# Kernel tuning notes

Hardware: AMD Instinct MI355X
Metric: run time of the kernel (lower is better)

## Reference

```python
import jax, jax.numpy as jnp
import numpy as np

N0, N1, N2 = 100000, 25000, 6250
F = 128
OUT = 5


def _mean_agg(feat_src, src, dst, n_dst):
    # DGL copy_u + mean: segment mean over destination nodes (0 for isolated dst)
    s = jax.ops.segment_sum(feat_src[src], dst, num_segments=n_dst)
    cnt = jax.ops.segment_sum(jnp.ones_like(dst, dtype=feat_src.dtype), dst, num_segments=n_dst)
    return s / jnp.maximum(cnt, 1.0)[:, None]


def _graph_conv(feat, src, dst, W, b, n):
    # DGL GraphConv, norm='both': D_src^-1/2 gather-sum D_dst^-1/2, then linear
    dt = feat.dtype
    out_deg = jax.ops.segment_sum(jnp.ones_like(src, dtype=dt), src, num_segments=n)
    in_deg = jax.ops.segment_sum(jnp.ones_like(dst, dtype=dt), dst, num_segments=n)
    ns = jnp.where(out_deg > 0, out_deg ** -0.5, 0.0)
    nd = jnp.where(in_deg > 0, in_deg ** -0.5, 0.0)
    agg = jax.ops.segment_sum((feat * ns[:, None])[src], dst, num_segments=n)
    return (agg * nd[:, None]) @ W + b


def setup_inputs() -> dict:
    key = jax.random.key(0)
    keys = jax.random.split(key, 64)
    _c = iter(range(64))
    def nrm(shape, s=0.05):
        return jax.random.normal(keys[next(_c)], shape, dtype=jnp.float32) * s
    def ri(n, hi):
        return jax.random.randint(keys[next(_c)], (n,), 0, hi)
    inp = {
        'X': nrm((N0, 32), 1.0),
        'g0_src': ri(1600000, N0), 'g0_dst': ri(1600000, N0),
        'g1_src': ri(400000, N1), 'g1_dst': ri(400000, N1),
        'g2_src': ri(100000, N2), 'g2_dst': ri(100000, N2),
        'inc0_src': ri(100000, N0), 'inc0_dst': ri(100000, N1),
        'inc1_src': ri(25000, N1), 'inc1_dst': ri(25000, N2),
        'dec0_src': ri(100000, N2), 'dec0_dst': ri(100000, N1),
        'dec1_src': ri(400000, N1), 'dec1_dst': ri(400000, N0),
        'W_emb': nrm((32, F)), 'b_emb': jnp.zeros((F,), jnp.float32),
        'W_gcn0': nrm((F, F)), 'b_gcn0': jnp.zeros((F,), jnp.float32),
        'W_gcn1': nrm((F, F)), 'b_gcn1': jnp.zeros((F,), jnp.float32),
        'W_gcn2': nrm((F, F)), 'b_gcn2': jnp.zeros((F,), jnp.float32),
        'W_enc0': nrm((F, F)), 'b_enc0': jnp.zeros((F,), jnp.float32),
        'W_enc1': nrm((F, F)), 'b_enc1': jnp.zeros((F,), jnp.float32),
        'W_dec0': nrm((F, F)), 'b_dec0': jnp.zeros((F,), jnp.float32),
        'W_dec1': nrm((F, F)), 'b_dec1': jnp.zeros((F,), jnp.float32),
        'W_head0': nrm((2 * F, OUT)), 'b_head0': jnp.zeros((OUT,), jnp.float32),
        'W_head1': nrm((2 * F, OUT)), 'b_head1': jnp.zeros((OUT,), jnp.float32),
        'W_head2': nrm((2 * F, OUT)), 'b_head2': jnp.zeros((OUT,), jnp.float32),
    }
    return inp


def reference(X, g0_src, g0_dst, g1_src, g1_dst, g2_src, g2_dst,
              inc0_src, inc0_dst, inc1_src, inc1_dst,
              dec0_src, dec0_dst, dec1_src, dec1_dst,
              W_emb, b_emb, W_gcn0, b_gcn0, W_gcn1, b_gcn1, W_gcn2, b_gcn2,
              W_enc0, b_enc0, W_enc1, b_enc1, W_dec0, b_dec0, W_dec1, b_dec1,
              W_head0, b_head0, W_head1, b_head1, W_head2, b_head2):
    # embedding at finest scale
    h0 = X @ W_emb + b_emb                                   # [N0, F]
    # encode + pool fine -> coarse (copy_u/mean)
    h1 = _mean_agg(h0 @ W_enc0 + b_enc0, inc0_src, inc0_dst, N1)   # [N1, F]
    h2 = _mean_agg(h1 @ W_enc1 + b_enc1, inc1_src, inc1_dst, N2)   # [N2, F]
    # intra-scale GraphConv
    g0 = _graph_conv(h0, g0_src, g0_dst, W_gcn0, b_gcn0, N0)
    g1 = _graph_conv(h1, g1_src, g1_dst, W_gcn1, b_gcn1, N1)
    g2 = _graph_conv(h2, g2_src, g2_dst, W_gcn2, b_gcn2, N2)
    # decode coarse -> fine
    d2 = g2
    d1 = _mean_agg(d2 @ W_dec0 + b_dec0, dec0_src, dec0_dst, N1)   # [N1, F]
    d0 = _mean_agg(d1 @ W_dec1 + b_dec1, dec1_src, dec1_dst, N0)   # [N0, F]
    # per-scale heads with softmax
    o0 = jax.nn.softmax(jnp.concatenate([g0, d0], -1) @ W_head0 + b_head0, axis=-1)
    o1 = jax.nn.softmax(jnp.concatenate([g1, d1], -1) @ W_head1 + b_head1, axis=-1)
    o2 = jax.nn.softmax(jnp.concatenate([g2, d2], -1) @ W_head2 + b_head2, axis=-1)
    return jnp.concatenate([o0, o1, o2], axis=0)             # [N0+N1+N2, OUT]
```

## Files before the change

### kernel.cpp

```cpp
#include <hip/hip_runtime.h>

#define F 128
static const int N0 = 100000, N1 = 25000, N2 = 6250;

typedef unsigned short u16;
typedef unsigned int   u32;
typedef __attribute__((ext_vector_type(8))) short bf16x8;
typedef __attribute__((ext_vector_type(4))) float f32x4;

__device__ __forceinline__ float bf2f(u16 u) {
    union { u32 i; float f; } v; v.i = ((u32)u) << 16; return v.f;
}
__device__ __forceinline__ u16 f2bf(float f) {
    u32 u = __float_as_uint(f);
    u += 0x7fff + ((u >> 16) & 1);
    return (u16)(u >> 16);
}

struct Seg7 {
    const int* src[7];
    const int* dst[7];
    int end[7];
    int cbase[7];
    int obase[7];
};
struct W7 { const float* w[7]; };

#define EPT 4
#define CEPT 8
#define SM32  (64*(32+8)*2 + 128*(32+8)*2 + 128*4)


__device__ __forceinline__ void dev_mm32(char* smem, const float* __restrict__ Ap,
                                         const float* __restrict__ W,
                                         const float* __restrict__ bias,
                                         u16* __restrict__ out, int M, int blk) {
    const int K = 32;
    const int KST = K + 8;
    u16* Al = (u16*)smem;
    u16* Wt = (u16*)(smem + 64 * KST * 2);
    float* bl = (float*)(smem + 64 * KST * 2 + 128 * KST * 2);
    int tid = threadIdx.x;
    int m0 = blk * 64;

    for (int i = tid; i < K * 128; i += 256) {
        int k = i >> 7, n = i & 127;
        Wt[n * KST + k] = f2bf(W[i]);
    }
    for (int i = tid; i < 64 * K; i += 256) {
        int r = i / K, c = i % K;
        int gr = m0 + r;
        Al[r * KST + c] = (gr < M) ? f2bf(Ap[(size_t)gr * K + c]) : (u16)0;
    }
    if (tid < 128) bl[tid] = bias[tid];
    __syncthreads();

    int w = tid >> 6, lane = tid & 63, m16 = lane & 15, quad = lane >> 4;
    f32x4 acc[8];
#pragma unroll
    for (int t = 0; t < 8; t++)
#pragma unroll
        for (int r = 0; r < 4; r++) acc[t][r] = 0.f;

    {
        bf16x8 af = *(const bf16x8*)&Al[(w * 16 + m16) * KST + quad * 8];
#pragma unroll
        for (int t = 0; t < 8; t++) {
            bf16x8 bf = *(const bf16x8*)&Wt[(t * 16 + m16) * KST + quad * 8];
            acc[t] = __builtin_amdgcn_mfma_f32_16x16x32_bf16(af, bf, acc[t], 0, 0, 0);
        }
    }
#pragma unroll
    for (int t = 0; t < 8; t++) {
#pragma unroll
        for (int r = 0; r < 4; r++) {
            int gr = m0 + w * 16 + quad * 4 + r;
            if (gr >= M) continue;
            int gc = t * 16 + m16;
            out[(size_t)gr * F + gc] = f2bf(acc[t][r] + bl[gc]);
        }
    }
}

template <bool MASK>
__device__ __forceinline__ void dev_mmd(const u16* __restrict__ Ap,
                                        const u16* __restrict__ Wtg,
                                        const float* __restrict__ bias,
                                        u16* __restrict__ out,
                                        const int* __restrict__ rowptr,
                                        int M, int blk) {
    int tid = threadIdx.x;
    int wv = tid >> 6, lane = tid & 63, m16 = lane & 15, quad = lane >> 4;
    int m0 = blk * 64;
    int arow = m0 + wv * 16 + m16;
    if (arow >= M) arow = M - 1;
    const u16* Arow = Ap + (size_t)arow * F;

    f32x4 acc[8];
#pragma unroll
    for (int t = 0; t < 8; t++)
#pragma unroll
        for (int r = 0; r < 4; r++) acc[t][r] = 0.f;

#pragma unroll
    for (int k0 = 0; k0 < F; k0 += 32) {
        bf16x8 af = *(const bf16x8*)&Arow[k0 + quad * 8];
#pragma unroll
        for (int t = 0; t < 8; t++) {
            bf16x8 bf = *(const bf16x8*)&Wtg[(t * 16 + m16) * F + k0 + quad * 8];
            acc[t] = __builtin_amdgcn_mfma_f32_16x16x32_bf16(af, bf, acc[t], 0, 0, 0);
        }
    }
#pragma unroll
    for (int t = 0; t < 8; t++) {
#pragma unroll
        for (int r = 0; r < 4; r++) {
            int gr = m0 + wv * 16 + quad * 4 + r;
            if (gr >= M) continue;
            int gc = t * 16 + m16;
            bool zrow = false;
            if (MASK) zrow = (rowptr[gr + 1] == rowptr[gr]);
            float v = acc[t][r] + bias[gc];
            out[(size_t)gr * F + gc] = zrow ? (u16)0 : f2bf(v);
        }
    }
}

template <int MODE>
__device__ __forceinline__ void dev_gather32(const u16* __restrict__ feat,
                                             const int* __restrict__ rowptr,
                                             const int* __restrict__ col,
                                             const int* __restrict__ od,
                                             u16* __restrict__ out, int M, int blk) {
    int row = (blk * 256 + (int)threadIdx.x) >> 5;
    if (row >= M) return;
    int l32 = threadIdx.x & 31;
    int fo = l32 << 2;
    int beg = rowptr[row], end = rowptr[row + 1];
    float a0 = 0.f, a1 = 0.f, a2 = 0.f, a3 = 0.f;
    int j = beg;
    for (; j + 8 <= end; j += 8) {
        int cc[8];
#pragma unroll
        for (int t = 0; t < 8; t++) cc[t] = col[j + t];
        float ss[8];
#pragma unroll
        for (int t = 0; t < 8; t++) {
            if (MODE == 1) { int o = od[cc[t]]; ss[t] = o > 0 ? rsqrtf((float)o) : 0.f; }
            else ss[t] = 1.f;
        }
        ushort4 uu[8];
#pragma unroll
        for (int t = 0; t < 8; t++) uu[t] = *(const ushort4*)&feat[(size_t)cc[t] * F + fo];
#pragma unroll
        for (int t = 0; t < 8; t++) {
            a0 += bf2f(uu[t].x) * ss[t]; a1 += bf2f(uu[t].y) * ss[t];
            a2 += bf2f(uu[t].z) * ss[t]; a3 += bf2f(uu[t].w) * ss[t];
        }
    }
    for (; j < end; j++) {
        int c = col[j];
        float s = 1.f;
        if (MODE == 1) { int o = od[c]; s = o > 0 ? rsqrtf((float)o) : 0.f; }
        ushort4 u = *(const ushort4*)&feat[(size_t)c * F + fo];
        a0 += bf2f(u.x) * s; a1 += bf2f(u.y) * s;
        a2 += bf2f(u.z) * s; a3 += bf2f(u.w) * s;
    }
    int deg = end - beg;
    float fs = (MODE == 0) ? (deg > 0 ? 1.f / (float)deg : 0.f)
                           : (deg > 0 ? rsqrtf((float)deg) : 0.f);
    ushort4 o;
    o.x = f2bf(a0 * fs); o.y = f2bf(a1 * fs);
    o.z = f2bf(a2 * fs); o.w = f2bf(a3 * fs);
    *(ushort4*)&out[(size_t)row * F + fo] = o;
}

template <bool GD>
__device__ __forceinline__ void dev_head(char* smem, const u16* __restrict__ g,
                                         const u16* __restrict__ d,
                                         const int* __restrict__ rowptr,
                                         const int* __restrict__ col,
                                         const float* __restrict__ Wh,
                                         const float* __restrict__ bh,
                                         float* __restrict__ out, int M, int blk) {
    float* Wl = (float*)smem;
    float* bl = (float*)(smem + 1280 * 4);
    int tid = threadIdx.x;
    for (int i = tid; i < 1280; i += 256) Wl[i] = Wh[i];
    if (tid < 5) bl[tid] = bh[tid];
    __syncthreads();

    int grp = tid >> 5;
    int l32 = tid & 31;
    int k0 = l32 << 2;
    for (int i = 0; i < 4; i++) {
        int row = blk * 32 + grp * 4 + i;
        if (row < M) {
            float dv[4];
            if (GD) {
                int beg = rowptr[row], end = rowptr[row + 1];
                dv[0] = dv[1] = dv[2] = dv[3] = 0.f;
                int j = beg;
                for (; j + 4 <= end; j += 4) {
                    int c0 = col[j], c1 = col[j + 1], c2 = col[j + 2], c3 = col[j + 3];
                    ushort4 u0 = *(const ushort4*)&d[(size_t)c0 * F + k0];
                    ushort4 u1 = *(const ushort4*)&d[(size_t)c1 * F + k0];
                    ushort4 u2 = *(const ushort4*)&d[(size_t)c2 * F + k0];
                    ushort4 u3 = *(const ushort4*)&d[(size_t)c3 * F + k0];
                    dv[0] += bf2f(u0.x) + bf2f(u1.x) + bf2f(u2.x) + bf2f(u3.x);
                    dv[1] += bf2f(u0.y) + bf2f(u1.y) + bf2f(u2.y) + bf2f(u3.y);
                    dv[2] += bf2f(u0.z) + bf2f(u1.z) + bf2f(u2.z) + bf2f(u3.z);
                    dv[3] += bf2f(u0.w) + bf2f(u1.w) + bf2f(u2.w) + bf2f(u3.w);
                }
                for (; j < end; j++) {
                    int c = col[j];
                    ushort4 u = *(const ushort4*)&d[(size_t)c * F + k0];
                    dv[0] += bf2f(u.x); dv[1] += bf2f(u.y);
                    dv[2] += bf2f(u.z); dv[3] += bf2f(u.w);
                }
                int deg = end - beg;
                float fs = deg > 0 ? 1.f / (float)deg : 0.f;
#pragma unroll
                for (int q = 0; q < 4; q++) dv[q] *= fs;
            } else {
                ushort4 du = *(const ushort4*)&d[(size_t)row * F + k0];
                dv[0] = bf2f(du.x); dv[1] = bf2f(du.y);
                dv[2] = bf2f(du.z); dv[3] = bf2f(du.w);
            }
            ushort4 gu = *(const ushort4*)&g[(size_t)row * F + k0];
            float gv[4] = {bf2f(gu.x), bf2f(gu.y), bf2f(gu.z), bf2f(gu.w)};
            float p[5];
#pragma unroll
            for (int o = 0; o < 5; o++) {
                float v = 0.f;
#pragma unroll
                for (int q = 0; q < 4; q++)
                    v += gv[q] * Wl[(k0 + q) * 5 + o] + dv[q] * Wl[(k0 + q + 128) * 5 + o];
                p[o] = v;
            }
#pragma unroll
            for (int o = 0; o < 5; o++) {
                float v = p[o];
                v += __shfl_xor(v, 16, 64);
                v += __shfl_xor(v, 8, 64);
                v += __shfl_xor(v, 4, 64);
                v += __shfl_xor(v, 2, 64);
                v += __shfl_xor(v, 1, 64);
                p[o] = v + bl[o];
            }
            if (l32 == 0) {
                float m = p[0];
#pragma unroll
                for (int o = 1; o < 5; o++) m = fmaxf(m, p[o]);
                float e[5], s = 0.f;
#pragma unroll
                for (int o = 0; o < 5; o++) { e[o] = expf(p[o] - m); s += e[o]; }
                float inv = 1.f / s;
#pragma unroll
                for (int o = 0; o < 5; o++) out[(size_t)row * 5 + o] = e[o] * inv;
            }
        }
    }
}


__global__ __launch_bounds__(256) void k_count_emb(Seg7 S, W7 Wsrc,
                                                   u16* __restrict__ WtAll,
                                                   int* __restrict__ cnt,
                                                   u16* __restrict__ occ, int ETOT,
                                                   const float* __restrict__ X,
                                                   const float* __restrict__ Wemb,
                                                   const float* __restrict__ bemb,
                                                   u16* __restrict__ h0,
                                                   int nbMM, int nbPrep) {
    __shared__ char smem[SM32];
    int blk = blockIdx.x;
    if (blk < nbMM) {
        dev_mm32(smem, X, Wemb, bemb, h0, N0, blk);
        return;
    }
    if (blk < nbMM + nbPrep) {
        int g = (blk - nbMM) * 256 + threadIdx.x;
        int m = g >> 14, idx = g & 16383;
        int n = idx >> 7, k = idx & 127;
        WtAll[g] = f2bf(Wsrc.w[m][k * 128 + n]);
        return;
    }
    int base = (blk - nbMM - nbPrep) * (256 * CEPT) + threadIdx.x;
    int ee[CEPT], grow[CEPT];
#pragma unroll
    for (int t = 0; t < CEPT; t++) {
        int e = base + t * 256;
        ee[t] = e;
        grow[t] = -1;
        if (e < ETOT) {
            int s = 0;
            while (e >= S.end[s]) s++;
            int le = e - ((s == 0) ? 0 : S.end[s - 1]);
            grow[t] = S.cbase[s] + S.dst[s][le];
        }
    }
    u32 r[CEPT];
#pragma unroll
    for (int t = 0; t < CEPT; t++)
        if (grow[t] >= 0) r[t] = atomicAdd((u32*)&cnt[grow[t]], 1u);
#pragma unroll
    for (int t = 0; t < CEPT; t++)
        if (grow[t] >= 0) occ[ee[t]] = (u16)r[t];
}

__global__ __launch_bounds__(256) void k_fill_od(Seg7 S,
                                                 const int* __restrict__ rowptr,
                                                 const u16* __restrict__ occ,
                                                 int* __restrict__ col,
                                                 int* __restrict__ od, int ETOT,
                                                 float invRow, float invOd) {
    int win = blockIdx.x & 7;
    int base = ((int)blockIdx.x >> 3) * (256 * EPT) + threadIdx.x;
#pragma unroll
    for (int t = 0; t < EPT; t++) {
        int e = base + t * 256;
        if (e >= ETOT) break;
        int s = 0;
        while (e >= S.end[s]) s++;
        int le = e - ((s == 0) ? 0 : S.end[s - 1]);
        int grow = S.cbase[s] + S.dst[s][le];
        int w1 = (int)((float)grow * invRow); w1 = w1 > 7 ? 7 : w1;
        int sv = -1;
        if (w1 == win || S.obase[s] >= 0) sv = S.src[s][le];
        if (w1 == win) col[rowptr[grow] + (int)occ[e]] = sv;
        if (S.obase[s] >= 0) {
            int gs = S.obase[s] + sv;
            int w2 = (int)((float)gs * invOd); w2 = w2 > 7 ? 7 : w2;
            if (w2 == win) atomicAdd(&od[gs], 1);
        }
    }
}

#define SCHUNK 4096
__global__ __launch_bounds__(1024) void k_scan1(const int* __restrict__ cnt,
                                                int* __restrict__ partial, int n) {
    __shared__ int red[1024];
    int tid = threadIdx.x;
    int base = blockIdx.x * SCHUNK + tid * 4;
    int s = 0;
#pragma unroll
    for (int j = 0; j < 4; j++) { int i = base + j; if (i < n) s += cnt[i]; }
    red[tid] = s;
    __syncthreads();
    for (int d = 512; d > 0; d >>= 1) {
        if (tid < d) red[tid] += red[tid + d];
        __syncthreads();
    }
    if (tid == 0) partial[blockIdx.x] = red[0];
}

__global__ __launch_bounds__(128) void k_scan2(int* __restrict__ partial, int G) {
    __shared__ int sh[128];
    int tid = threadIdx.x;
    sh[tid] = (tid < G) ? partial[tid] : 0;
    __syncthreads();
    for (int d = 1; d < 128; d <<= 1) {
        int t = (tid >= d) ? sh[tid - d] : 0;
        __syncthreads();
        sh[tid] += t;
        __syncthreads();
    }
    if (tid < G) partial[tid] = (tid > 0) ? sh[tid - 1] : 0;
    if (tid == 127) partial[G] = sh[127];
}

__global__ __launch_bounds__(1024) void k_scan3(const int* __restrict__ cnt,
                                                const int* __restrict__ partial,
                                                int* __restrict__ rowptr,
                                                int n, int G) {
    __shared__ int red[1024];
    int tid = threadIdx.x;
    int base = blockIdx.x * SCHUNK + tid * 4;
    int v0 = 0, v1 = 0, v2 = 0, v3 = 0;
    if (base + 0 < n) v0 = cnt[base + 0];
    if (base + 1 < n) v1 = cnt[base + 1];
    if (base + 2 < n) v2 = cnt[base + 2];
    if (base + 3 < n) v3 = cnt[base + 3];
    red[tid] = v0 + v1 + v2 + v3;
    __syncthreads();
    for (int d = 1; d < 1024; d <<= 1) {
        int t = (tid >= d) ? red[tid - d] : 0;
        __syncthreads();
        red[tid] += t;
        __syncthreads();
    }
    int off = partial[blockIdx.x] + ((tid > 0) ? red[tid - 1] : 0);
    if (base + 0 < n) { rowptr[base + 0] = off; off += v0; }
    if (base + 1 < n) { rowptr[base + 1] = off; off += v1; }
    if (base + 2 < n) { rowptr[base + 2] = off; off += v2; }
    if (base + 3 < n) { rowptr[base + 3] = off; off += v3; }
    if (blockIdx.x == 0 && tid == 0) rowptr[n] = partial[G];
}

template <int MODE>
__global__ __launch_bounds__(256) void k_g32(const u16* __restrict__ feat,
                                             const int* __restrict__ rowptr,
                                             const int* __restrict__ col,
                                             const int* __restrict__ od,
                                             u16* __restrict__ out, int M) {
    dev_gather32<MODE>(feat, rowptr, col, od, out, M, blockIdx.x);
}

template <int MA, int MB>
__global__ __launch_bounds__(256) void k_g32x2(
    const u16* fA, const int* rpA, const int* oA, u16* outA, int MAr, int nbA,
    const u16* fB, const int* rpB, const int* oB, u16* outB, int MBr,
    const int* __restrict__ col) {
    if ((int)blockIdx.x < nbA) dev_gather32<MA>(fA, rpA, col, oA, outA, MAr, blockIdx.x);
    else                       dev_gather32<MB>(fB, rpB, col, oB, outB, MBr, blockIdx.x - nbA);
}

template <bool MASK>
__global__ __launch_bounds__(256) void k_mmd(const u16* __restrict__ Ap,
                                             const u16* __restrict__ Wtg,
                                             const float* __restrict__ bias,
                                             u16* __restrict__ out,
                                             const int* __restrict__ rowptr, int M) {
    dev_mmd<MASK>(Ap, Wtg, bias, out, rowptr, M, blockIdx.x);
}

__global__ __launch_bounds__(256) void k_mmd2(
    const u16* A1, const u16* Wt1, const float* b1, u16* o1, const int* rp1, int M1, int nb1,
    const u16* A2, const u16* Wt2, const float* b2, u16* o2, int M2) {
    if ((int)blockIdx.x < nb1) dev_mmd<true >(A1, Wt1, b1, o1, rp1, M1, blockIdx.x);
    else                       dev_mmd<false>(A2, Wt2, b2, o2, nullptr, M2, blockIdx.x - nb1);
}

__global__ __launch_bounds__(256) void k_mmd_g32(
    const u16* A1, const u16* Wt1, const float* b1, u16* o1, const int* rp1, int M1, int nb1,
    const u16* feat, const int* rp2, const int* od2, u16* out2, int M2,
    const int* __restrict__ col) {
    if ((int)blockIdx.x < nb1) dev_mmd<true>(A1, Wt1, b1, o1, rp1, M1, blockIdx.x);
    else dev_gather32<1>(feat, rp2, col, od2, out2, M2, blockIdx.x - nb1);
}

__global__ __launch_bounds__(256) void k_g32_mmd(
    const u16* feat, const int* rp1, const int* od1, u16* out1, int M1, int nb1,
    const u16* A2, const u16* Wt2, const float* b2, u16* o2, int M2,
    const int* __restrict__ col) {
    if ((int)blockIdx.x < nb1) dev_gather32<1>(feat, rp1, col, od1, out1, M1, blockIdx.x);
    else dev_mmd<false>(A2, Wt2, b2, o2, nullptr, M2, blockIdx.x - nb1);
}

__global__ __launch_bounds__(256) void k_head3(
    const u16* Ga, const u16* dFeat, const int* rpD1, const int* colp,
    const float* Wa, const float* Ba, int nb0,
    const u16* Gb, const u16* Db, const float* Wb, const float* Bb, int nb1,
    const u16* Gc, const float* Wc, const float* Bc,
    float* __restrict__ out) {
    __shared__ char smem[1280 * 4 + 32];
    int b = blockIdx.x;
    if (b < nb0)            dev_head<true >(smem, Ga, dFeat, rpD1, colp, Wa, Ba, out, N0, b);
    else if (b < nb0 + nb1) dev_head<false>(smem, Gb, Db, nullptr, nullptr, Wb, Bb, out + (size_t)N0 * 5, N1, b - nb0);
    else                    dev_head<false>(smem, Gc, Gc, nullptr, nullptr, Wc, Bc, out + (size_t)(N0 + N1) * 5, N2, b - nb0 - nb1);
}

extern "C" void kernel_launch(void* const* d_in, const int* in_sizes, int n_in,
                              void* d_out, int out_size, void* d_ws, size_t ws_size,
                              hipStream_t stream) {
    const float* X = (const float*)d_in[0];
    const int *g0s = (const int*)d_in[1], *g0d = (const int*)d_in[2];
    const int *g1s = (const int*)d_in[3], *g1d = (const int*)d_in[4];
    const int *g2s = (const int*)d_in[5], *g2d = (const int*)d_in[6];
    const int *i0s = (const int*)d_in[7], *i0d = (const int*)d_in[8];
    const int *i1s = (const int*)d_in[9], *i1d = (const int*)d_in[10];
    const int *dc0s = (const int*)d_in[11], *dc0d = (const int*)d_in[12];
    const int *dc1s = (const int*)d_in[13], *dc1d = (const int*)d_in[14];
    const float *Wemb = (const float*)d_in[15], *bemb = (const float*)d_in[16];
    const float *Wg0 = (const float*)d_in[17], *bg0 = (const float*)d_in[18];
    const float *Wg1 = (const float*)d_in[19], *bg1 = (const float*)d_in[20];
    const float *Wg2 = (const float*)d_in[21], *bg2 = (const float*)d_in[22];
    const float *We0 = (const float*)d_in[23], *be0 = (const float*)d_in[24];
    const float *We1 = (const float*)d_in[25], *be1 = (const float*)d_in[26];
    const float *Wd0 = (const float*)d_in[27], *bd0 = (const float*)d_in[28];
    const float *Wd1 = (const float*)d_in[29], *bd1 = (const float*)d_in[30];
    const float *Wh0 = (const float*)d_in[31], *bh0 = (const float*)d_in[32];
    const float *Wh1 = (const float*)d_in[33], *bh1 = (const float*)d_in[34];
    const float *Wh2 = (const float*)d_in[35], *bh2 = (const float*)d_in[36];
    const int Eg0 = in_sizes[1], Eg1 = in_sizes[3], Eg2 = in_sizes[5];
    const int Ei0 = in_sizes[7], Ei1 = in_sizes[9];
    const int Ed0 = in_sizes[11], Ed1 = in_sizes[13];
    (void)n_in; (void)out_size; (void)ws_size;

    const int B_I0 = 0;
    const int B_I1 = B_I0 + N1;
    const int B_G2 = B_I1 + N2;
    const int B_D0 = B_G2 + N2;
    const int B_G1 = B_D0 + N1;
    const int B_G0 = B_G1 + N1;
    const int B_D1 = B_G0 + N0;
    const int NROWS = B_D1 + N0;
    const int ETOT  = Eg0 + Eg1 + Eg2 + Ei0 + Ei1 + Ed0 + Ed1;
    const int OB_G0 = 0, OB_G1 = N0, OB_G2 = N0 + N1;
    const int NOD = N0 + N1 + N2;
    const int G = (NROWS + SCHUNK - 1) / SCHUNK;
    const int rowsPerWin = (NROWS + 7) / 8;
    const int odPerWin   = (NOD + 7) / 8;
    const float invRow = 1.0f / (float)rowsPerWin;
    const float invOd  = 1.0f / (float)odPerWin;
    const int NCH = (ETOT + 256 * EPT - 1) / (256 * EPT);

    char* wsb = (char*)d_ws;
    size_t off = 0;
    auto alloc = [&](size_t bytes) -> char* {
        char* p = wsb + off;
        off = (off + bytes + 255) & ~(size_t)255;
        return p;
    };
    u16* h0  = (u16*)alloc((size_t)N0 * F * 2);
    u16* h1  = (u16*)alloc((size_t)N1 * F * 2);
    u16* h2  = (u16*)alloc((size_t)N2 * F * 2);
    u16* G0  = (u16*)alloc((size_t)N0 * F * 2);
    u16* G1  = (u16*)alloc((size_t)N1 * F * 2);
    u16* G2  = (u16*)alloc((size_t)N2 * F * 2);
    u16* D1  = (u16*)alloc((size_t)N1 * F * 2);
    u16* agg = (u16*)alloc((size_t)N0 * F * 2);
    u16* bN1 = (u16*)alloc((size_t)N1 * F * 2);
    u16* bN2 = (u16*)alloc((size_t)N2 * F * 2);
    u16* pA  = D1;
    u16* WtAll = (u16*)alloc((size_t)7 * 16384 * 2);
    int* cnt    = (int*)alloc((size_t)NROWS * 4);
    int* od     = (int*)alloc((size_t)NOD * 4);
    int* rowptr = (int*)alloc((size_t)(NROWS + 1) * 4);
    u16* occ    = (u16*)alloc((size_t)ETOT * 2);
    int* col    = (int*)alloc((size_t)ETOT * 4);
    int* part   = (int*)alloc((size_t)(G + 1) * 4);
    float* out = (float*)d_out;

    u16* WtE0 = WtAll + 0 * 16384;
    u16* WtG0 = WtAll + 1 * 16384;
    u16* WtE1 = WtAll + 2 * 16384;
    u16* WtG1 = WtAll + 3 * 16384;
    u16* WtG2 = WtAll + 4 * 16384;
    u16* WtD0 = WtAll + 5 * 16384;
    u16* WtD1 = WtAll + 6 * 16384;
    W7 Wsrc;
    Wsrc.w[0] = We0; Wsrc.w[1] = Wg0; Wsrc.w[2] = We1; Wsrc.w[3] = Wg1;
    Wsrc.w[4] = Wg2; Wsrc.w[5] = Wd0; Wsrc.w[6] = Wd1;

    Seg7 S;
    S.src[0] = i0s;  S.dst[0] = i0d;  S.cbase[0] = B_I0; S.obase[0] = -1;
    S.src[1] = i1s;  S.dst[1] = i1d;  S.cbase[1] = B_I1; S.obase[1] = -1;
    S.src[2] = g2s;  S.dst[2] = g2d;  S.cbase[2] = B_G2; S.obase[2] = OB_G2;
    S.src[3] = dc0s; S.dst[3] = dc0d; S.cbase[3] = B_D0; S.obase[3] = -1;
    S.src[4] = g1s;  S.dst[4] = g1d;  S.cbase[4] = B_G1; S.obase[4] = OB_G1;
    S.src[5] = g0s;  S.dst[5] = g0d;  S.cbase[5] = B_G0; S.obase[5] = OB_G0;
    S.src[6] = dc1s; S.dst[6] = dc1d; S.cbase[6] = B_D1; S.obase[6] = -1;
    {
        int Es[7] = {Ei0, Ei1, Eg2, Ed0, Eg1, Eg0, Ed1};
        int acc = 0;
        for (int i = 0; i < 7; i++) { acc += Es[i]; S.end[i] = acc; }
    }

    const int nbEmb   = (N0 + 63) / 64;
    const int nbPrep  = (7 * 16384) / 256;
    const int nbCount = (ETOT + 256 * CEPT - 1) / (256 * CEPT);
    const int nbFill  = NCH * 8;

    hipMemsetAsync(cnt, 0, (size_t)((char*)od - (char*)cnt) + (size_t)NOD * 4, stream);
    k_count_emb<<<nbEmb + nbPrep + nbCount, 256, 0, stream>>>(
        S, Wsrc, WtAll, cnt, occ, ETOT, X, Wemb, bemb, h0, nbEmb, nbPrep);
    k_scan1<<<G, 1024, 0, stream>>>(cnt, part, NROWS);
    k_scan2<<<1, 128, 0, stream>>>(part, G);
    k_scan3<<<G, 1024, 0, stream>>>(cnt, part, rowptr, NROWS, G);
    k_fill_od<<<nbFill, 256, 0, stream>>>(S, rowptr, occ, col, od, ETOT, invRow, invOd);

    k_g32<0><<<(N1 * 32 + 255) / 256, 256, 0, stream>>>(h0, rowptr + B_I0, col, nullptr, pA, N1);
    {
        int nb1 = (N1 + 63) / 64;
        int nb2 = (N0 * 32 + 255) / 256;
        k_mmd_g32<<<nb1 + nb2, 256, 0, stream>>>(pA, WtE0, be0, h1, rowptr + B_I0, N1, nb1,
                                                 h0, rowptr + B_G0, od + OB_G0, agg, N0, col);
    }
    {
        int nbA = (N2 * 32 + 255) / 256, nbB = (N1 * 32 + 255) / 256;
        k_g32x2<0, 1><<<nbA + nbB, 256, 0, stream>>>(
            h1, rowptr + B_I1, nullptr, bN2, N2, nbA,
            h1, rowptr + B_G1, od + OB_G1, bN1, N1, col);
    }
    {
        int nb1 = (N2 + 63) / 64, nb2 = (N1 + 63) / 64;
        k_mmd2<<<nb1 + nb2, 256, 0, stream>>>(bN2, WtE1, be1, h2, rowptr + B_I1, N2, nb1,
                                              bN1, WtG1, bg1, G1, N1);
    }
    {
        int nb1 = (N2 * 32 + 255) / 256;
        int nb2 = (N0 + 63) / 64;
        k_g32_mmd<<<nb1 + nb2, 256, 0, stream>>>(h2, rowptr + B_G2, od + OB_G2, bN2, N2, nb1,
                                                 agg, WtG0, bg0, G0, N0, col);
    }
    k_mmd<false><<<(N2 + 63) / 64, 256, 0, stream>>>(bN2, WtG2, bg2, G2, nullptr, N2);
    k_mmd<false><<<(N2 + 63) / 64, 256, 0, stream>>>(G2, WtD0, bd0, bN2, nullptr, N2);
    k_g32<0><<<(N1 * 32 + 255) / 256, 256, 0, stream>>>(bN2, rowptr + B_D0, col, nullptr, D1, N1);
    k_mmd<false><<<(N1 + 63) / 64, 256, 0, stream>>>(D1, WtD1, bd1, bN1, nullptr, N1);
    {
        int nb0 = (N0 + 31) / 32, nb1 = (N1 + 31) / 32, nb2 = (N2 + 31) / 32;
        k_head3<<<nb0 + nb1 + nb2, 256, 0, stream>>>(G0, bN1, rowptr + B_D1, col, Wh0, bh0, nb0,
                                                     G1, D1, Wh1, bh1, nb1,
                                                     G2, Wh2, bh2, out);
    }
}
```

Baseline: 680.9 us.

## Move out-degree counting into count kernel and fuse chained N2 matmuls

Out-degree atomics for the three GraphConv graphs move from the windowed fill kernel into extra blocks of the count/embedding kernel. The fill kernel then only scatters column indices and skips the src reads and window filtering for od. A new k_mmdd kernel runs the two back-to-back N2 matmuls (gcn2 then dec0) in one launch, keeping the intermediate tile in shared memory. This saves one launch and one global round trip, at the cost of a separate pN2 buffer and unwindowed od atomics.

```diff
diff --git a/kernel.cpp b/kernel.cpp
--- a/kernel.cpp
+++ b/kernel.cpp
@@ -22,12 +22,17 @@
     const int* dst[7];
     int end[7];
     int cbase[7];
-    int obase[7];
+};
+struct SegO {
+    const int* src[3];
+    int end[3];
+    int obase[3];
 };
 struct W7 { const float* w[7]; };
 
 #define EPT 4
 #define CEPT 8
+#define AST (F + 8)
 #define SM32  (64*(32+8)*2 + 128*(32+8)*2 + 128*4)
 
 
@@ -264,15 +269,17 @@
 }
 
 
-__global__ __launch_bounds__(256) void k_count_emb(Seg7 S, W7 Wsrc,
+__global__ __launch_bounds__(256) void k_count_emb(Seg7 S, SegO SO, W7 Wsrc,
                                                    u16* __restrict__ WtAll,
                                                    int* __restrict__ cnt,
-                                                   u16* __restrict__ occ, int ETOT,
+                                                   int* __restrict__ od,
+                                                   u16* __restrict__ occ,
+                                                   int ETOT, int ETOTG,
                                                    const float* __restrict__ X,
                                                    const float* __restrict__ Wemb,
                                                    const float* __restrict__ bemb,
                                                    u16* __restrict__ h0,
-                                                   int nbMM, int nbPrep) {
+                                                   int nbMM, int nbPrep, int nbCnt) {
     __shared__ char smem[SM32];
     int blk = blockIdx.x;
     if (blk < nbMM) {
@@ -286,35 +293,53 @@
         WtAll[g] = f2bf(Wsrc.w[m][k * 128 + n]);
         return;
     }
-    int base = (blk - nbMM - nbPrep) * (256 * CEPT) + threadIdx.x;
-    int ee[CEPT], grow[CEPT];
+    if (blk < nbMM + nbPrep + nbCnt) {
+        int base = (blk - nbMM - nbPrep) * (256 * CEPT) + threadIdx.x;
+        int ee[CEPT], grow[CEPT];
+#pragma unroll
+        for (int t = 0; t < CEPT; t++) {
+            int e = base + t * 256;
+            ee[t] = e;
+            grow[t] = -1;
+            if (e < ETOT) {
+                int s = 0;
+                while (e >= S.end[s]) s++;
+                int le = e - ((s == 0) ? 0 : S.end[s - 1]);
+                grow[t] = S.cbase[s] + S.dst[s][le];
+            }
+        }
+        u32 r[CEPT];
+#pragma unroll
+        for (int t = 0; t < CEPT; t++)
+            if (grow[t] >= 0) r[t] = atomicAdd((u32*)&cnt[grow[t]], 1u);
+#pragma unroll
+        for (int t = 0; t < CEPT; t++)
+            if (grow[t] >= 0) occ[ee[t]] = (u16)r[t];
+        return;
+    }
+    int base = (blk - nbMM - nbPrep - nbCnt) * (256 * CEPT) + threadIdx.x;
+    int gs[CEPT];
 #pragma unroll
     for (int t = 0; t < CEPT; t++) {
         int e = base + t * 256;
-        ee[t] = e;
-        grow[t] = -1;
-        if (e < ETOT) {
+        gs[t] = -1;
+        if (e < ETOTG) {
             int s = 0;
-            while (e >= S.end[s]) s++;
-            int le = e - ((s == 0) ? 0 : S.end[s - 1]);
-            grow[t] = S.cbase[s] + S.dst[s][le];
-        }
-    }
-    u32 r[CEPT];
+            while (e >= SO.end[s]) s++;
+            int le = e - ((s == 0) ? 0 : SO.end[s - 1]);
+            gs[t] = SO.obase[s] + SO.src[s][le];
+        }
+    }
 #pragma unroll
     for (int t = 0; t < CEPT; t++)
-        if (grow[t] >= 0) r[t] = atomicAdd((u32*)&cnt[grow[t]], 1u);
-#pragma unroll
-    for (int t = 0; t < CEPT; t++)
-        if (grow[t] >= 0) occ[ee[t]] = (u16)r[t];
-}
-
-__global__ __launch_bounds__(256) void k_fill_od(Seg7 S,
-                                                 const int* __restrict__ rowptr,
-                                                 const u16* __restrict__ occ,
-                                                 int* __restrict__ col,
-                                                 int* __restrict__ od, int ETOT,
-                                                 float invRow, float invOd) {
+        if (gs[t] >= 0) atomicAdd(&od[gs[t]], 1);
+}
+
+__global__ __launch_bounds__(256) void k_fill(Seg7 S,
+                                              const int* __restrict__ rowptr,
+                                              const u16* __restrict__ occ,
+                                              int* __restrict__ col, int ETOT,
+                                              float invRow) {
     int win = blockIdx.x & 7;
     int base = ((int)blockIdx.x >> 3) * (256 * EPT) + threadIdx.x;
 #pragma unroll
@@ -326,14 +351,7 @@
         int le = e - ((s == 0) ? 0 : S.end[s - 1]);
         int grow = S.cbase[s] + S.dst[s][le];
         int w1 = (int)((float)grow * invRow); w1 = w1 > 7 ? 7 : w1;
-        int sv = -1;
-        if (w1 == win || S.obase[s] >= 0) sv = S.src[s][le];
-        if (w1 == win) col[rowptr[grow] + (int)occ[e]] = sv;
-        if (S.obase[s] >= 0) {
-            int gs = S.obase[s] + sv;
-            int w2 = (int)((float)gs * invOd); w2 = w2 > 7 ? 7 : w2;
-            if (w2 == win) atomicAdd(&od[gs], 1);
-        }
+        if (w1 == win) col[rowptr[grow] + (int)occ[e]] = S.src[s][le];
     }
 }
 
@@ -430,6 +448,74 @@
     const u16* A2, const u16* Wt2, const float* b2, u16* o2, int M2) {
     if ((int)blockIdx.x < nb1) dev_mmd<true >(A1, Wt1, b1, o1, rp1, M1, blockIdx.x);
     else                       dev_mmd<false>(A2, Wt2, b2, o2, nullptr, M2, blockIdx.x - nb1);
+}
+
+__global__ __launch_bounds__(256) void k_mmdd(const u16* __restrict__ Ap,
+                                              const u16* __restrict__ Wt1,
+                                              const float* __restrict__ b1,
+                                              u16* __restrict__ out1,
+                                              const u16* __restrict__ Wt2,
+                                              const float* __restrict__ b2,
+                                              u16* __restrict__ out2, int M) {
+    __shared__ u16 Gl[64 * AST];
+    int tid = threadIdx.x;
+    int wv = tid >> 6, lane = tid & 63, m16 = lane & 15, quad = lane >> 4;
+    int m0 = (int)blockIdx.x * 64;
+    int arow = m0 + wv * 16 + m16;
+    if (arow >= M) arow = M - 1;
+    const u16* Arow = Ap + (size_t)arow * F;
+
+    f32x4 acc[8];
+#pragma unroll
+    for (int t = 0; t < 8; t++)
+#pragma unroll
+        for (int r = 0; r < 4; r++) acc[t][r] = 0.f;
+#pragma unroll
+    for (int k0 = 0; k0 < F; k0 += 32) {
+        bf16x8 af = *(const bf16x8*)&Arow[k0 + quad * 8];
+#pragma unroll
+        for (int t = 0; t < 8; t++) {
+            bf16x8 bf = *(const bf16x8*)&Wt1[(t * 16 + m16) * F + k0 + quad * 8];
+            acc[t] = __builtin_amdgcn_mfma_f32_16x16x32_bf16(af, bf, acc[t], 0, 0, 0);
+        }
+    }
+#pragma unroll
+    for (int t = 0; t < 8; t++) {
+#pragma unroll
+        for (int r = 0; r < 4; r++) {
+            int lr = wv * 16 + quad * 4 + r;
+            int gr = m0 + lr;
+            int gc = t * 16 + m16;
+            u16 v = f2bf(acc[t][r] + b1[gc]);
+            Gl[lr * AST + gc] = v;
+            if (gr < M) out1[(size_t)gr * F + gc] = v;
+        }
+    }
+    __syncthreads();
+
+#pragma unroll
+    for (int t = 0; t < 8; t++)
+#pragma unroll
+        for (int r = 0; r < 4; r++) acc[t][r] = 0.f;
+#pragma unroll
+    for (int k0 = 0; k0 < F; k0 += 32) {
+        bf16x8 af = *(const bf16x8*)&Gl[(wv * 16 + m16) * AST + k0 + quad * 8];
+#pragma unroll
+        for (int t = 0; t < 8; t++) {
+            bf16x8 bf = *(const bf16x8*)&Wt2[(t * 16 + m16) * F + k0 + quad * 8];
+            acc[t] = __builtin_amdgcn_mfma_f32_16x16x32_bf16(af, bf, acc[t], 0, 0, 0);
+        }
+    }
+#pragma unroll
+    for (int t = 0; t < 8; t++) {
+#pragma unroll
+        for (int r = 0; r < 4; r++) {
+            int gr = m0 + wv * 16 + quad * 4 + r;
+            if (gr >= M) continue;
+            int gc = t * 16 + m16;
+            out2[(size_t)gr * F + gc] = f2bf(acc[t][r] + b2[gc]);
+        }
+    }
 }
 
 __global__ __launch_bounds__(256) void k_mmd_g32(
@@ -497,13 +583,12 @@
     const int B_D1 = B_G0 + N0;
     const int NROWS = B_D1 + N0;
     const int ETOT  = Eg0 + Eg1 + Eg2 + Ei0 + Ei1 + Ed0 + Ed1;
+    const int ETOTG = Eg0 + Eg1 + Eg2;
     const int OB_G0 = 0, OB_G1 = N0, OB_G2 = N0 + N1;
     const int NOD = N0 + N1 + N2;
     const int G = (NROWS + SCHUNK - 1) / SCHUNK;
     const int rowsPerWin = (NROWS + 7) / 8;
-    const int odPerWin   = (NOD + 7) / 8;
     const float invRow = 1.0f / (float)rowsPerWin;
-    const float invOd  = 1.0f / (float)odPerWin;
     const int NCH = (ETOT + 256 * EPT - 1) / (256 * EPT);
 
     char* wsb = (char*)d_ws;
@@ -523,6 +608,7 @@
     u16* agg = (u16*)alloc((size_t)N0 * F * 2);
     u16* bN1 = (u16*)alloc((size_t)N1 * F * 2);
     u16* bN2 = (u16*)alloc((size_t)N2 * F * 2);
+    u16* pN2 = (u16*)alloc((size_t)N2 * F * 2);
     u16* pA  = D1;
     u16* WtAll = (u16*)alloc((size_t)7 * 16384 * 2);
     int* cnt    = (int*)alloc((size_t)NROWS * 4);
@@ -545,31 +631,37 @@
     Wsrc.w[4] = Wg2; Wsrc.w[5] = Wd0; Wsrc.w[6] = Wd1;
 
     Seg7 S;
-    S.src[0] = i0s;  S.dst[0] = i0d;  S.cbase[0] = B_I0; S.obase[0] = -1;
-    S.src[1] = i1s;  S.dst[1] = i1d;  S.cbase[1] = B_I1; S.obase[1] = -1;
-    S.src[2] = g2s;  S.dst[2] = g2d;  S.cbase[2] = B_G2; S.obase[2] = OB_G2;
-    S.src[3] = dc0s; S.dst[3] = dc0d; S.cbase[3] = B_D0; S.obase[3] = -1;
-    S.src[4] = g1s;  S.dst[4] = g1d;  S.cbase[4] = B_G1; S.obase[4] = OB_G1;
-    S.src[5] = g0s;  S.dst[5] = g0d;  S.cbase[5] = B_G0; S.obase[5] = OB_G0;
-    S.src[6] = dc1s; S.dst[6] = dc1d; S.cbase[6] = B_D1; S.obase[6] = -1;
+    S.src[0] = i0s;  S.dst[0] = i0d;  S.cbase[0] = B_I0;
+    S.src[1] = i1s;  S.dst[1] = i1d;  S.cbase[1] = B_I1;
+    S.src[2] = g2s;  S.dst[2] = g2d;  S.cbase[2] = B_G2;
+    S.src[3] = dc0s; S.dst[3] = dc0d; S.cbase[3] = B_D0;
+    S.src[4] = g1s;  S.dst[4] = g1d;  S.cbase[4] = B_G1;
+    S.src[5] = g0s;  S.dst[5] = g0d;  S.cbase[5] = B_G0;
+    S.src[6] = dc1s; S.dst[6] = dc1d; S.cbase[6] = B_D1;
     {
         int Es[7] = {Ei0, Ei1, Eg2, Ed0, Eg1, Eg0, Ed1};
         int acc = 0;
         for (int i = 0; i < 7; i++) { acc += Es[i]; S.end[i] = acc; }
     }
+    SegO SO;
+    SO.src[0] = g0s; SO.obase[0] = OB_G0; SO.end[0] = Eg0;
+    SO.src[1] = g1s; SO.obase[1] = OB_G1; SO.end[1] = Eg0 + Eg1;
+    SO.src[2] = g2s; SO.obase[2] = OB_G2; SO.end[2] = Eg0 + Eg1 + Eg2;
 
     const int nbEmb   = (N0 + 63) / 64;
     const int nbPrep  = (7 * 16384) / 256;
-    const int nbCount = (ETOT + 256 * CEPT - 1) / (256 * CEPT);
+    const int nbCnt   = (ETOT + 256 * CEPT - 1) / (256 * CEPT);
+    const int nbOd    = (ETOTG + 256 * CEPT - 1) / (256 * CEPT);
     const int nbFill  = NCH * 8;
 
     hipMemsetAsync(cnt, 0, (size_t)((char*)od - (char*)cnt) + (size_t)NOD * 4, stream);
-    k_count_emb<<<nbEmb + nbPrep + nbCount, 256, 0, stream>>>(
-        S, Wsrc, WtAll, cnt, occ, ETOT, X, Wemb, bemb, h0, nbEmb, nbPrep);
+    k_count_emb<<<nbEmb + nbPrep + nbCnt + nbOd, 256, 0, stream>>>(
+        S, SO, Wsrc, WtAll, cnt, od, occ, ETOT, ETOTG, X, Wemb, bemb, h0,
+        nbEmb, nbPrep, nbCnt);
     k_scan1<<<G, 1024, 0, stream>>>(cnt, part, NROWS);
     k_scan2<<<1, 128, 0, stream>>>(part, G);
     k_scan3<<<G, 1024, 0, stream>>>(cnt, part, rowptr, NROWS, G);
-    k_fill_od<<<nbFill, 256, 0, stream>>>(S, rowptr, occ, col, od, ETOT, invRow, invOd);
+    k_fill<<<nbFill, 256, 0, stream>>>(S, rowptr, occ, col, ETOT, invRow);
 
     k_g32<0><<<(N1 * 32 + 255) / 256, 256, 0, stream>>>(h0, rowptr + B_I0, col, nullptr, pA, N1);
     {
@@ -595,9 +687,8 @@
         k_g32_mmd<<<nb1 + nb2, 256, 0, stream>>>(h2, rowptr + B_G2, od + OB_G2, bN2, N2, nb1,
                                                  agg, WtG0, bg0, G0, N0, col);
     }
-    k_mmd<false><<<(N2 + 63) / 64, 256, 0, stream>>>(bN2, WtG2, bg2, G2, nullptr, N2);
-    k_mmd<false><<<(N2 + 63) / 64, 256, 0, stream>>>(G2, WtD0, bd0, bN2, nullptr, N2);
-    k_g32<0><<<(N1 * 32 + 255) / 256, 256, 0, stream>>>(bN2, rowptr + B_D0, col, nullptr, D1, N1);
+    k_mmdd<<<(N2 + 63) / 64, 256, 0, stream>>>(bN2, WtG2, bg2, G2, WtD0, bd0, pN2, N2);
+    k_g32<0><<<(N1 * 32 + 255) / 256, 256, 0, stream>>>(pN2, rowptr + B_D0, col, nullptr, D1, N1);
     k_mmd<false><<<(N1 + 63) / 64, 256, 0, stream>>>(D1, WtD1, bd1, bN1, nullptr, N1);
     {
         int nb0 = (N0 + 31) / 32, nb1 = (N1 + 31) / 32, nb2 = (N2 + 31) / 32;
```

After: 744.3 us. +9.3%, slower.
